# Performance work log

Hardware: AMD Instinct MI355X
Metric: run time of the kernel (lower is better)

Reference implementation:

```python
import jax, jax.numpy as jnp
import numpy as np

B, N, NFEAT, NHID, NOUT, H = 16, 1024, 128, 256, 256, 4
DH = NOUT // H  # 64 per head
EPS = 1e-5
ALPHA = 0.2  # LeakyReLU negative slope


def setup_inputs() -> dict:
    key = jax.random.key(0)
    ks = jax.random.split(key, 8)
    stdv = 1.0 / np.sqrt(NHID)
    return {
        "x": jax.random.normal(ks[0], (B, N, NFEAT), dtype=jnp.float32),
        "adj": jax.random.uniform(ks[1], (N, N), dtype=jnp.float32) / N,
        "gc_w": jax.random.uniform(ks[2], (NFEAT, NHID), minval=-stdv, maxval=stdv, dtype=jnp.float32),
        "gc_b": jax.random.uniform(ks[3], (NHID,), minval=-stdv, maxval=stdv, dtype=jnp.float32),
        "bn1_gamma": jnp.ones((NHID,), jnp.float32),
        "bn1_beta": jnp.zeros((NHID,), jnp.float32),
        "gat_w": jax.random.normal(ks[4], (H, NHID, DH), dtype=jnp.float32) * (1.0 / np.sqrt(NHID)),
        "conv_w": jax.random.normal(ks[5], (NOUT, NOUT, 3), dtype=jnp.float32) * (1.0 / np.sqrt(NOUT * 3)),
        "conv_b": jnp.zeros((NOUT,), jnp.float32),
        "bn2_gamma": jnp.ones((NOUT,), jnp.float32),
        "bn2_beta": jnp.zeros((NOUT,), jnp.float32),
    }


def reference(x, adj, gc_w, gc_b, bn1_gamma, bn1_beta, gat_w, conv_w, conv_b, bn2_gamma, bn2_beta):
    # --- GraphConvolution: adj @ (x @ W) + b, relu ---
    h = jnp.einsum("bnf,fo->bno", x, gc_w)
    h = jnp.einsum("nm,bmo->bno", adj, h) + gc_b
    h = jax.nn.relu(h)
    # --- BatchNorm1d over channel dim (training-mode batch stats), relu ---
    mu = h.mean((0, 1))
    var = h.var((0, 1))
    h = (h - mu) * jax.lax.rsqrt(var + EPS) * bn1_gamma + bn1_beta
    h = jax.nn.relu(h)
    # --- Multi-head GAT: per head hp, e = hp hp^T, leakyrelu, softmax, attn @ hp ---
    hp = jnp.einsum("bnf,hfd->bhnd", h, gat_w)          # (B,H,N,DH)
    e = jnp.einsum("bhnd,bhmd->bhnm", hp, hp)            # (B,H,N,N)
    e = jnp.where(e > 0, e, ALPHA * e)
    attn = jax.nn.softmax(e, axis=-1)
    out = jnp.einsum("bhnm,bhmd->bhnd", attn, hp)        # = sum_m attn * hp (the B,N,N,d repeat in torch)
    out = out.transpose(0, 2, 1, 3).reshape(B, N, H * DH)  # concat heads -> (B,N,NOUT)
    # --- TCN block: conv1d (k=3, pad 1) over node axis, batchnorm, relu (dropout=eval) ---
    xc = out.transpose(0, 2, 1)                          # (B,C,N)
    y = jax.lax.conv_general_dilated(xc, conv_w, (1,), [(1, 1)],
                                     dimension_numbers=("NCH", "OIH", "NCH"))
    y = y + conv_b[None, :, None]
    mu2 = y.mean((0, 2), keepdims=True)
    var2 = y.var((0, 2), keepdims=True)
    y = (y - mu2) * jax.lax.rsqrt(var2 + EPS) * bn2_gamma[None, :, None] + bn2_beta[None, :, None]
    y = jax.nn.relu(y)
    return y.transpose(0, 2, 1)                          # (B,N,NOUT)
```

## Files before the change

kernel.cpp:

```cpp
#include <hip/hip_runtime.h>
#include <hip/hip_bf16.h>


typedef unsigned short u16;
typedef __attribute__((ext_vector_type(8))) short short8;
typedef __attribute__((ext_vector_type(4))) float f32x4;

static __device__ __forceinline__ float4 ld4(const float* p){ return *(const float4*)p; }
static __device__ __forceinline__ void st4(float* p, float4 v){ *(float4*)p = v; }

static __device__ __forceinline__ u16 f2bf(float f){
  unsigned u = __builtin_bit_cast(unsigned, f);
  unsigned r = u + 0x7FFFu + ((u >> 16) & 1u);
  return (u16)(r >> 16);
}
static __device__ __forceinline__ float bf2f(u16 h){
  unsigned u = ((unsigned)h) << 16; return __builtin_bit_cast(float, u);
}
static __device__ __forceinline__ void st4bf(u16* p, u16 a, u16 b, u16 c, u16 d){
  uint2 v; v.x = (unsigned)a | ((unsigned)b << 16); v.y = (unsigned)c | ((unsigned)d << 16);
  *(uint2*)p = v;
}
static __device__ __forceinline__ f32x4 mfma16(short8 a, short8 b, f32x4 c){
  return __builtin_amdgcn_mfma_f32_16x16x32_bf16(a, b, c, 0, 0, 0);
}

template<int SPLIT, int K, int NN, int MODE, int AXSWAP, int BM, int BN, int WR, int WC>
static __device__ __forceinline__ void mgemm_body(
    const u16* __restrict__ Ah_, const u16* __restrict__ Al_,
    const u16* __restrict__ Bh_, const u16* __restrict__ Bl_,
    const u16* __restrict__ zbuf,
    void* __restrict__ C0v, void* __restrict__ C1v, void* __restrict__ C2v,
    const float* __restrict__ bias)
{
  constexpr int KT = K / 32;
  constexpr int WM = BM / WR, WN = BN / WC;
  constexpr int MI = WM / 16, NJ = WN / 16;
  __shared__ u16 Ah[BM * 32], Bh[BN * 32];
  __shared__ u16 Al[SPLIT == 3 ? BM * 32 : 8], Bl[SPLIT == 3 ? BN * 32 : 8];
  const int tid = threadIdx.x;
  const int n0 = (AXSWAP ? blockIdx.y : blockIdx.x) * BN;
  const int m0 = (AXSWAP ? blockIdx.x : blockIdx.y) * BM;
  const int lane = tid & 63, l15 = lane & 15, lq = lane >> 4;
  const int w = tid >> 6, wr = w / WC, wc = w % WC;

  f32x4 acc[MI][NJ] = {};

  for (int kt = 0; kt < KT; ++kt){
    const int k0 = kt * 32;
#pragma unroll
    for (int r = 0; r < BM / 64; ++r){
      const int slot = r * 256 + tid;
      const int row = slot & (BM - 1), kh = slot / BM;
      const int ldsoff = (r * 256 + (tid & 192)) * 8;
      const u16* asrc;
      if constexpr (MODE == 3){
        const int kz = k0 >> 8;
        const int ci0 = (k0 & 255) + kh * 8;
        const int R = m0 + row;
        const int nn = (R & 1023) + kz - 1;
        asrc = ((unsigned)nn < 1024u) ? (Ah_ + (size_t)(R + kz - 1) * 256 + ci0) : zbuf;
      } else {
        asrc = Ah_ + (size_t)(m0 + row) * K + k0 + kh * 8;
      }
      __builtin_amdgcn_global_load_lds(asrc, &Ah[ldsoff], 16, 0, 0);
      if constexpr (SPLIT == 3){
        const u16* asrc2 = Al_ + (size_t)(m0 + row) * K + k0 + kh * 8;
        __builtin_amdgcn_global_load_lds(asrc2, &Al[ldsoff], 16, 0, 0);
      }
    }
#pragma unroll
    for (int r = 0; r < BN / 64; ++r){
      const int slot = r * 256 + tid;
      const int row = slot & (BN - 1), kh = slot / BN;
      const int ldsoff = (r * 256 + (tid & 192)) * 8;
      const u16* bsrc = Bh_ + (size_t)(n0 + row) * K + k0 + kh * 8;
      __builtin_amdgcn_global_load_lds(bsrc, &Bh[ldsoff], 16, 0, 0);
      if constexpr (SPLIT == 3){
        const u16* bsrc2 = Bl_ + (size_t)(n0 + row) * K + k0 + kh * 8;
        __builtin_amdgcn_global_load_lds(bsrc2, &Bl[ldsoff], 16, 0, 0);
      }
    }
    __syncthreads();
    short8 afh[MI], bfh[NJ], afl[MI], bfl[NJ];
#pragma unroll
    for (int f = 0; f < MI; ++f){
      afh[f] = *(const short8*)&Ah[(lq * BM + wr * WM + f * 16 + l15) * 8];
      if constexpr (SPLIT == 3)
        afl[f] = *(const short8*)&Al[(lq * BM + wr * WM + f * 16 + l15) * 8];
    }
#pragma unroll
    for (int f = 0; f < NJ; ++f){
      bfh[f] = *(const short8*)&Bh[(lq * BN + wc * WN + f * 16 + l15) * 8];
      if constexpr (SPLIT == 3)
        bfl[f] = *(const short8*)&Bl[(lq * BN + wc * WN + f * 16 + l15) * 8];
    }
#pragma unroll
    for (int fi = 0; fi < MI; ++fi)
#pragma unroll
      for (int fj = 0; fj < NJ; ++fj){
        acc[fi][fj] = mfma16(afh[fi], bfh[fj], acc[fi][fj]);
        if constexpr (SPLIT == 3){
          acc[fi][fj] = mfma16(afl[fi], bfh[fj], acc[fi][fj]);
          acc[fi][fj] = mfma16(afh[fi], bfl[fj], acc[fi][fj]);
        }
      }
    __syncthreads();
  }

  const int rb = m0 + wr * WM;
  const int cb = n0 + wc * WN;
  if constexpr (MODE == 0){
    u16* H = (u16*)C0v; u16* L = (u16*)C1v;
#pragma unroll
    for (int fi = 0; fi < MI; ++fi){
      const int R = rb + fi * 16 + lq * 4;
      const int nn = R & 1023, bq = R >> 10;
#pragma unroll
      for (int fj = 0; fj < NJ; ++fj){
        const int c = cb + fj * 16 + l15;
        const size_t off = (size_t)(bq * 256 + c) * 1024 + nn;
        u16 h_[4], l_[4];
#pragma unroll
        for (int r = 0; r < 4; ++r){
          float v = acc[fi][fj][r];
          u16 hi = f2bf(v); h_[r] = hi; l_[r] = f2bf(v - bf2f(hi));
        }
        st4bf(H + off, h_[0], h_[1], h_[2], h_[3]);
        st4bf(L + off, l_[0], l_[1], l_[2], l_[3]);
      }
    }
  } else if constexpr (MODE == 1){
    u16* GH = (u16*)C0v; u16* GL = (u16*)C1v; float* PT = (float*)C2v;
    const int mb = AXSWAP ? blockIdx.x : blockIdx.y;
#pragma unroll
    for (int fj = 0; fj < NJ; ++fj){
      const int c = cb + fj * 16 + l15;
      const int o = c & 255, bq = c >> 8;
      const float bs = bias[o];
      float s = 0.f, q = 0.f;
#pragma unroll
      for (int fi = 0; fi < MI; ++fi){
        const int R = rb + fi * 16 + lq * 4;
#pragma unroll
        for (int r = 0; r < 4; ++r){
          const float v = fmaxf(acc[fi][fj][r] + bs, 0.f);
          s += v; q = fmaf(v, v, q);
          const u16 hi = f2bf(v);
          const size_t off = ((size_t)bq * 1024 + R + r) * 256 + o;
          GH[off] = hi;
          GL[off] = f2bf(v - bf2f(hi));
        }
      }
      s += __shfl_xor(s, 16, 64); s += __shfl_xor(s, 32, 64);
      q += __shfl_xor(q, 16, 64); q += __shfl_xor(q, 32, 64);
      if (lq == 0){
        PT[mb * 4096 + c]         = s;
        PT[65536 + mb * 4096 + c] = q;
      }
    }
  } else if constexpr (MODE == 2){
    u16* H = (u16*)C0v; u16* L = (u16*)C1v; u16* T = (u16*)C2v;
#pragma unroll
    for (int fi = 0; fi < MI; ++fi){
      const int R = rb + fi * 16 + lq * 4;
#pragma unroll
      for (int fj = 0; fj < NJ; ++fj){
        const int c = cb + fj * 16 + l15;
        u16 h_[4];
#pragma unroll
        for (int r = 0; r < 4; ++r){
          float v = acc[fi][fj][r];
          u16 hi = f2bf(v); h_[r] = hi;
          H[(size_t)(R + r) * 256 + c] = hi;
          L[(size_t)(R + r) * 256 + c] = f2bf(v - bf2f(hi));
        }
        st4bf(T + (size_t)c * 16384 + R, h_[0], h_[1], h_[2], h_[3]);
      }
    }
  } else {
    float* Y = (float*)C0v; float* PT = (float*)C2v;
    const int slot = blockIdx.y * 2 + wr;
#pragma unroll
    for (int fj = 0; fj < NJ; ++fj){
      const int c = cb + fj * 16 + l15;
      const float bs = bias[c];
      float s = 0.f, q = 0.f;
#pragma unroll
      for (int fi = 0; fi < MI; ++fi){
        const int R = rb + fi * 16 + lq * 4;
#pragma unroll
        for (int r = 0; r < 4; ++r){
          const float v = acc[fi][fj][r] + bs;
          s += v; q = fmaf(v, v, q);
          Y[(size_t)(R + r) * 256 + c] = v;
        }
      }
      s += __shfl_xor(s, 16, 64); s += __shfl_xor(s, 32, 64);
      q += __shfl_xor(q, 16, 64); q += __shfl_xor(q, 32, 64);
      if (lq == 0){
        PT[slot * 256 + c]         = s;
        PT[65536 + slot * 256 + c] = q;
      }
    }
  }
}

__global__ __launch_bounds__(256) void gemm0_k(
    const u16* __restrict__ Ah_, const u16* __restrict__ Bh_,
    const u16* __restrict__ zbuf, void* __restrict__ C0, void* __restrict__ C1)
{ mgemm_body<1, 128, 256, 0, 0, 128, 64, 2, 2>(Ah_, nullptr, Bh_, nullptr, zbuf, C0, C1, nullptr, nullptr); }

__global__ __launch_bounds__(256) void gemm1_k(
    const u16* __restrict__ Ah_, const u16* __restrict__ Al_,
    const u16* __restrict__ Bh_, const u16* __restrict__ Bl_,
    const u16* __restrict__ zbuf, void* __restrict__ C0, void* __restrict__ C1,
    void* __restrict__ C2, const float* __restrict__ bias)
{ mgemm_body<3, 1024, 4096, 1, 1, 64, 128, 1, 4>(Ah_, Al_, Bh_, Bl_, zbuf, C0, C1, C2, bias); }

__global__ __launch_bounds__(256) void gemm2_k(
    const u16* __restrict__ Ah_, const u16* __restrict__ Al_,
    const u16* __restrict__ Bh_, const u16* __restrict__ Bl_,
    const u16* __restrict__ zbuf,
    void* __restrict__ C0, void* __restrict__ C1, void* __restrict__ C2)
{ mgemm_body<3, 256, 256, 2, 0, 128, 64, 2, 2>(Ah_, Al_, Bh_, Bl_, zbuf, C0, C1, C2, nullptr); }

__global__ __launch_bounds__(256) void gemm3_k(
    const u16* __restrict__ Ah_, const u16* __restrict__ Bh_,
    const u16* __restrict__ zbuf, void* __restrict__ C0, void* __restrict__ C2,
    const float* __restrict__ bias)
{ mgemm_body<1, 768, 256, 3, 0, 128, 64, 2, 2>(Ah_, nullptr, Bh_, nullptr, zbuf, C0, nullptr, C2, bias); }

__global__ __launch_bounds__(256) void flash(
    const u16* __restrict__ hp_hi, const u16* __restrict__ hp_lo,
    const u16* __restrict__ hpT, u16* __restrict__ ao)
{
  __shared__ u16 Khi[4096], Klo[4096], Vt[4096];
  __shared__ u16 Pl[4][2048];
  __shared__ float Ls[4][32];
  const int tid = threadIdx.x;
  const int lane = tid & 63, l15 = lane & 15, lq = lane >> 4, w = tid >> 6;
  const int bid = blockIdx.x;
  const int b = bid & 15, k_ = bid >> 4, h = k_ >> 3, qo = k_ & 7;
  const size_t qrow0 = (size_t)b * 1024 + qo * 128 + w * 32;

  short8 qh[2][2], ql[2][2];
#pragma unroll
  for (int mf = 0; mf < 2; ++mf)
#pragma unroll
    for (int ks = 0; ks < 2; ++ks){
      const size_t off = (qrow0 + mf * 16 + l15) * 256 + h * 64 + ks * 32 + lq * 8;
      qh[mf][ks] = *(const short8*)(hp_hi + off);
      ql[mf][ks] = *(const short8*)(hp_lo + off);
    }

  f32x4 o_[4][2] = {};
  float ls[8] = {};

  for (int kt = 0; kt < 16; ++kt){
    const int kv0 = kt * 64;
#pragma unroll
    for (int r = 0; r < 2; ++r){
      const int slot = r * 256 + tid;
      const int g1 = slot >> 6, g2 = slot & 63;
      const int ldsoff = (r * 256 + (tid & 192)) * 8;
      const u16* ksrc = hp_hi + ((size_t)b * 1024 + kv0 + g2) * 256 + h * 64 + g1 * 8;
      __builtin_amdgcn_global_load_lds(ksrc, &Khi[ldsoff], 16, 0, 0);
      const u16* ksrc2 = hp_lo + ((size_t)b * 1024 + kv0 + g2) * 256 + h * 64 + g1 * 8;
      __builtin_amdgcn_global_load_lds(ksrc2, &Klo[ldsoff], 16, 0, 0);
      const u16* vsrc = hpT + (size_t)(h * 64 + g2) * 16384 + b * 1024 + kv0 + g1 * 8;
      __builtin_amdgcn_global_load_lds(vsrc, &Vt[ldsoff], 16, 0, 0);
    }
    __syncthreads();

#pragma unroll
    for (int nf = 0; nf < 4; ++nf){
      short8 kf[2], kg[2];
#pragma unroll
      for (int ks = 0; ks < 2; ++ks){
        kf[ks] = *(const short8*)&Khi[((ks * 4 + lq) * 64 + nf * 16 + l15) * 8];
        kg[ks] = *(const short8*)&Klo[((ks * 4 + lq) * 64 + nf * 16 + l15) * 8];
      }
      const int kv = nf * 16 + l15;
#pragma unroll
      for (int mf = 0; mf < 2; ++mf){
        f32x4 s = {};
#pragma unroll
        for (int ks = 0; ks < 2; ++ks){
          s = mfma16(qh[mf][ks], kf[ks], s);
          s = mfma16(ql[mf][ks], kf[ks], s);
          s = mfma16(qh[mf][ks], kg[ks], s);
        }
        const int qb = mf * 16 + lq * 4;
        const int base = ((kv >> 3) * 32 + qb) * 8 + (kv & 7);
#pragma unroll
        for (int r = 0; r < 4; ++r){
          float v = s[r];
          v = v > 0.f ? v : 0.2f * v;
          const float p = __expf(v - 40.f);
          ls[mf * 4 + r] += p;
          Pl[w][base + r * 8] = f2bf(p);
        }
      }
    }

#pragma unroll
    for (int ks = 0; ks < 2; ++ks){
      short8 va[4], pf[2];
#pragma unroll
      for (int f = 0; f < 4; ++f)
        va[f] = *(const short8*)&Vt[((ks * 4 + lq) * 64 + f * 16 + l15) * 8];
#pragma unroll
      for (int f = 0; f < 2; ++f)
        pf[f] = *(const short8*)&Pl[w][((ks * 4 + lq) * 32 + f * 16 + l15) * 8];
#pragma unroll
      for (int df = 0; df < 4; ++df)
#pragma unroll
        for (int qf = 0; qf < 2; ++qf)
          o_[df][qf] = mfma16(va[df], pf[qf], o_[df][qf]);
    }
    __syncthreads();
  }

#pragma unroll
  for (int mask = 1; mask < 16; mask <<= 1)
#pragma unroll
    for (int i = 0; i < 8; ++i)
      ls[i] += __shfl_xor(ls[i], mask, 64);
  if (l15 == 0){
#pragma unroll
    for (int mf = 0; mf < 2; ++mf)
#pragma unroll
      for (int r = 0; r < 4; ++r)
        Ls[w][mf * 16 + lq * 4 + r] = ls[mf * 4 + r];
  }
  __syncthreads();
  float inv[2];
#pragma unroll
  for (int qf = 0; qf < 2; ++qf) inv[qf] = 1.0f / Ls[w][qf * 16 + l15];

#pragma unroll
  for (int qf = 0; qf < 2; ++qf)
#pragma unroll
    for (int df = 0; df < 4; ++df){
      const size_t addr = (qrow0 + qf * 16 + l15) * 256 + h * 64 + df * 16 + lq * 4;
      st4bf(ao + addr,
            f2bf(o_[df][qf][0] * inv[qf]), f2bf(o_[df][qf][1] * inv[qf]),
            f2bf(o_[df][qf][2] * inv[qf]), f2bf(o_[df][qf][3] * inv[qf]));
    }
}

__global__ __launch_bounds__(256) void bn_final(const float* __restrict__ part,
                                                const float* __restrict__ gamma,
                                                const float* __restrict__ beta,
                                                float* __restrict__ prm)
{
  const int t = threadIdx.x;
  float s = 0.f, q = 0.f;
#pragma unroll 8
  for (int i = 0; i < 256; ++i){ s += part[i * 256 + t]; q += part[65536 + i * 256 + t]; }
  const float mu = s * (1.f / 16384.f);
  const float var = q * (1.f / 16384.f) - mu * mu;
  prm[t] = mu;
  prm[256 + t] = rsqrtf(var + 1e-5f) * gamma[t];
  prm[512 + t] = beta[t];
}

__global__ __launch_bounds__(256) void bn_apply_split(
    const u16* __restrict__ GH, const u16* __restrict__ GL,
    u16* __restrict__ H, u16* __restrict__ L, const float* __restrict__ prm)
{
  const int idx = blockIdx.x * 256 + threadIdx.x;
  const size_t off = (size_t)idx * 4;
  const int o = (int)(off & 255);
  const uint2 hv = *(const uint2*)(GH + off);
  const uint2 lv = *(const uint2*)(GL + off);
  const float4 m = ld4(prm + o), rs = ld4(prm + 256 + o), bt = ld4(prm + 512 + o);
  float x0 = bf2f((u16)(hv.x & 0xffff)) + bf2f((u16)(lv.x & 0xffff));
  float x1 = bf2f((u16)(hv.x >> 16))    + bf2f((u16)(lv.x >> 16));
  float x2 = bf2f((u16)(hv.y & 0xffff)) + bf2f((u16)(lv.y & 0xffff));
  float x3 = bf2f((u16)(hv.y >> 16))    + bf2f((u16)(lv.y >> 16));
  u16 h_[4], l_[4];
  float v;
  v = fmaxf(fmaf(x0 - m.x, rs.x, bt.x), 0.f); h_[0] = f2bf(v); l_[0] = f2bf(v - bf2f(h_[0]));
  v = fmaxf(fmaf(x1 - m.y, rs.y, bt.y), 0.f); h_[1] = f2bf(v); l_[1] = f2bf(v - bf2f(h_[1]));
  v = fmaxf(fmaf(x2 - m.z, rs.z, bt.z), 0.f); h_[2] = f2bf(v); l_[2] = f2bf(v - bf2f(h_[2]));
  v = fmaxf(fmaf(x3 - m.w, rs.w, bt.w), 0.f); h_[3] = f2bf(v); l_[3] = f2bf(v - bf2f(h_[3]));
  st4bf(H + off, h_[0], h_[1], h_[2], h_[3]);
  st4bf(L + off, l_[0], l_[1], l_[2], l_[3]);
}

__global__ __launch_bounds__(256) void bn_apply(const float* __restrict__ in,
                                                float* __restrict__ outp,
                                                const float* __restrict__ prm)
{
  const int idx = blockIdx.x * 256 + threadIdx.x;
  const size_t off = (size_t)idx * 8;
  const int o = (int)(off & 255);
  const float4 x0 = ld4(in + off),      x1 = ld4(in + off + 4);
  const float4 m0 = ld4(prm + o),       m1 = ld4(prm + o + 4);
  const float4 r0 = ld4(prm + 256 + o), r1 = ld4(prm + 256 + o + 4);
  const float4 b0 = ld4(prm + 512 + o), b1 = ld4(prm + 512 + o + 4);
  float4 y0, y1;
  y0.x = fmaxf(fmaf(x0.x - m0.x, r0.x, b0.x), 0.f);
  y0.y = fmaxf(fmaf(x0.y - m0.y, r0.y, b0.y), 0.f);
  y0.z = fmaxf(fmaf(x0.z - m0.z, r0.z, b0.z), 0.f);
  y0.w = fmaxf(fmaf(x0.w - m0.w, r0.w, b0.w), 0.f);
  y1.x = fmaxf(fmaf(x1.x - m1.x, r1.x, b1.x), 0.f);
  y1.y = fmaxf(fmaf(x1.y - m1.y, r1.y, b1.y), 0.f);
  y1.z = fmaxf(fmaf(x1.z - m1.z, r1.z, b1.z), 0.f);
  y1.w = fmaxf(fmaf(x1.w - m1.w, r1.w, b1.w), 0.f);
  st4(outp + off, y0);
  st4(outp + off + 4, y1);
}

__global__ __launch_bounds__(256) void pack_w(
    const float* __restrict__ x, const float* __restrict__ adj,
    const float* __restrict__ gcw, const float* __restrict__ gatw,
    const float* __restrict__ convw,
    u16* __restrict__ xbf, u16* __restrict__ adjh, u16* __restrict__ adjl,
    u16* __restrict__ w0t, u16* __restrict__ w2th, u16* __restrict__ w2tl,
    u16* __restrict__ cwt, u16* __restrict__ zb)
{
  const int idx = blockIdx.x * 256 + threadIdx.x;
  if (idx < 2097152) xbf[idx] = f2bf(x[idx]);
  if (idx < 1048576){
    const float v = adj[idx];
    const u16 hi = f2bf(v);
    adjh[idx] = hi; adjl[idx] = f2bf(v - bf2f(hi));
  }
  if (idx < 32768){
    const int o = idx >> 7, f = idx & 127;
    w0t[idx] = f2bf(gcw[f * 256 + o]);
  }
  if (idx < 65536){
    const int c = idx >> 8, f = idx & 255;
    const float v = gatw[(c >> 6) * 16384 + f * 64 + (c & 63)];
    const u16 hi = f2bf(v);
    w2th[idx] = hi; w2tl[idx] = f2bf(v - bf2f(hi));
  }
  if (idx < 196608){
    const int co = idx / 768, k = idx - co * 768;
    const int kz = k >> 8, ci = k & 255;
    cwt[idx] = f2bf(convw[co * 768 + ci * 3 + kz]);
  }
  if (idx < 2048) zb[idx] = 0;
}

extern "C" void kernel_launch(void* const* d_in, const int* in_sizes, int n_in,
                              void* d_out, int out_size, void* d_ws, size_t ws_size,
                              hipStream_t stream)
{
  const float* x     = (const float*)d_in[0];
  const float* adj   = (const float*)d_in[1];
  const float* gc_w  = (const float*)d_in[2];
  const float* gc_b  = (const float*)d_in[3];
  const float* bn1g  = (const float*)d_in[4];
  const float* bn1b  = (const float*)d_in[5];
  const float* gatw  = (const float*)d_in[6];
  const float* convw = (const float*)d_in[7];
  const float* convb = (const float*)d_in[8];
  const float* bn2g  = (const float*)d_in[9];
  const float* bn2b  = (const float*)d_in[10];
  char* ws  = (char*)d_ws;
  char* out = (char*)d_out;

  u16* h1t_hi = (u16*)(ws + 0);
  u16* h1t_lo = (u16*)(ws + 8388608);
  u16* x_bf   = (u16*)(ws + 16777216);
  u16* adj_hi = (u16*)(ws + 20971520);
  u16* adj_lo = (u16*)(ws + 23068672);
  u16* hpT    = (u16*)(ws + 16777216);
  u16* w0t    = (u16*)(ws + 25165824);
  u16* w2th   = (u16*)(ws + 25231360);
  u16* w2tl   = (u16*)(ws + 25362432);
  u16* cwt    = (u16*)(ws + 25493504);
  u16* zbuf   = (u16*)(ws + 25886720);
  float* P1   = (float*)(ws + 25890816);
  float* PR1  = (float*)(ws + 26415104);
  float* PR2  = (float*)(ws + 26419200);
  u16* h_hi  = (u16*)(ws + 0);
  u16* h_lo  = (u16*)(ws + 8388608);
  u16* ao    = (u16*)(ws + 0);
  u16* g_hi  = (u16*)out;
  u16* g_lo  = (u16*)(out + 8388608);
  u16* hp_hi = (u16*)out;
  u16* hp_lo = (u16*)(out + 8388608);
  float* y   = (float*)out;

  pack_w<<<8192, 256, 0, stream>>>(x, adj, gc_w, gatw, convw,
                                   x_bf, adj_hi, adj_lo, w0t, w2th, w2tl, cwt, zbuf);
  gemm0_k<<<dim3(4, 128), 256, 0, stream>>>(x_bf, w0t, zbuf, h1t_hi, h1t_lo);
  gemm1_k<<<dim3(16, 32), 256, 0, stream>>>(adj_hi, adj_lo, h1t_hi, h1t_lo, zbuf,
                                            g_hi, g_lo, P1, gc_b);
  bn_final<<<1, 256, 0, stream>>>(P1, bn1g, bn1b, PR1);
  bn_apply_split<<<4096, 256, 0, stream>>>(g_hi, g_lo, h_hi, h_lo, PR1);
  gemm2_k<<<dim3(4, 128), 256, 0, stream>>>(h_hi, h_lo, w2th, w2tl, zbuf, hp_hi, hp_lo, hpT);
  flash<<<512, 256, 0, stream>>>(hp_hi, hp_lo, hpT, ao);
  gemm3_k<<<dim3(4, 128), 256, 0, stream>>>(ao, cwt, zbuf, y, P1, convb);
  bn_final<<<1, 256, 0, stream>>>(P1, bn2g, bn2b, PR2);
  bn_apply<<<2048, 256, 0, stream>>>(y, y, PR2);
}
```

Measured before the change: 301.5 us.

## Double-buffer LDS tiles in GEMM and flash-attention kernels with MFMA priority hints

```diff
diff --git a/kernel.cpp b/kernel.cpp
--- a/kernel.cpp
+++ b/kernel.cpp
@@ -36,8 +36,8 @@
   constexpr int KT = K / 32;
   constexpr int WM = BM / WR, WN = BN / WC;
   constexpr int MI = WM / 16, NJ = WN / 16;
-  __shared__ u16 Ah[BM * 32], Bh[BN * 32];
-  __shared__ u16 Al[SPLIT == 3 ? BM * 32 : 8], Bl[SPLIT == 3 ? BN * 32 : 8];
+  __shared__ u16 Ah[2][BM * 32], Bh[2][BN * 32];
+  __shared__ u16 Al[2][SPLIT == 3 ? BM * 32 : 8], Bl[2][SPLIT == 3 ? BN * 32 : 8];
   const int tid = threadIdx.x;
   const int n0 = (AXSWAP ? blockIdx.y : blockIdx.x) * BN;
   const int m0 = (AXSWAP ? blockIdx.x : blockIdx.y) * BM;
@@ -46,7 +46,7 @@
 
   f32x4 acc[MI][NJ] = {};
 
-  for (int kt = 0; kt < KT; ++kt){
+  auto STAGE = [&](int buf, int kt){
     const int k0 = kt * 32;
 #pragma unroll
     for (int r = 0; r < BM / 64; ++r){
@@ -63,10 +63,10 @@
       } else {
         asrc = Ah_ + (size_t)(m0 + row) * K + k0 + kh * 8;
       }
-      __builtin_amdgcn_global_load_lds(asrc, &Ah[ldsoff], 16, 0, 0);
+      __builtin_amdgcn_global_load_lds(asrc, &Ah[buf][ldsoff], 16, 0, 0);
       if constexpr (SPLIT == 3){
         const u16* asrc2 = Al_ + (size_t)(m0 + row) * K + k0 + kh * 8;
-        __builtin_amdgcn_global_load_lds(asrc2, &Al[ldsoff], 16, 0, 0);
+        __builtin_amdgcn_global_load_lds(asrc2, &Al[buf][ldsoff], 16, 0, 0);
       }
     }
 #pragma unroll
@@ -75,25 +75,31 @@
       const int row = slot & (BN - 1), kh = slot / BN;
       const int ldsoff = (r * 256 + (tid & 192)) * 8;
       const u16* bsrc = Bh_ + (size_t)(n0 + row) * K + k0 + kh * 8;
-      __builtin_amdgcn_global_load_lds(bsrc, &Bh[ldsoff], 16, 0, 0);
+      __builtin_amdgcn_global_load_lds(bsrc, &Bh[buf][ldsoff], 16, 0, 0);
       if constexpr (SPLIT == 3){
         const u16* bsrc2 = Bl_ + (size_t)(n0 + row) * K + k0 + kh * 8;
-        __builtin_amdgcn_global_load_lds(bsrc2, &Bl[ldsoff], 16, 0, 0);
-      }
-    }
-    __syncthreads();
+        __builtin_amdgcn_global_load_lds(bsrc2, &Bl[buf][ldsoff], 16, 0, 0);
+      }
+    }
+  };
+
+  STAGE(0, 0);
+  __syncthreads();
+  for (int kt = 0; kt < KT; ++kt){
+    const int cur = kt & 1;
+    if (kt + 1 < KT) STAGE(cur ^ 1, kt + 1);
     short8 afh[MI], bfh[NJ], afl[MI], bfl[NJ];
 #pragma unroll
     for (int f = 0; f < MI; ++f){
-      afh[f] = *(const short8*)&Ah[(lq * BM + wr * WM + f * 16 + l15) * 8];
+      afh[f] = *(const short8*)&Ah[cur][(lq * BM + wr * WM + f * 16 + l15) * 8];
       if constexpr (SPLIT == 3)
-        afl[f] = *(const short8*)&Al[(lq * BM + wr * WM + f * 16 + l15) * 8];
+        afl[f] = *(const short8*)&Al[cur][(lq * BM + wr * WM + f * 16 + l15) * 8];
     }
 #pragma unroll
     for (int f = 0; f < NJ; ++f){
-      bfh[f] = *(const short8*)&Bh[(lq * BN + wc * WN + f * 16 + l15) * 8];
+      bfh[f] = *(const short8*)&Bh[cur][(lq * BN + wc * WN + f * 16 + l15) * 8];
       if constexpr (SPLIT == 3)
-        bfl[f] = *(const short8*)&Bl[(lq * BN + wc * WN + f * 16 + l15) * 8];
+        bfl[f] = *(const short8*)&Bl[cur][(lq * BN + wc * WN + f * 16 + l15) * 8];
     }
 #pragma unroll
     for (int fi = 0; fi < MI; ++fi)
@@ -235,9 +241,8 @@
     const u16* __restrict__ hp_hi, const u16* __restrict__ hp_lo,
     const u16* __restrict__ hpT, u16* __restrict__ ao)
 {
-  __shared__ u16 Khi[4096], Klo[4096], Vt[4096];
+  __shared__ u16 Khi[2][4096], Klo[2][4096], Vt[2][4096];
   __shared__ u16 Pl[4][2048];
-  __shared__ float Ls[4][32];
   const int tid = threadIdx.x;
   const int lane = tid & 63, l15 = lane & 15, lq = lane >> 4, w = tid >> 6;
   const int bid = blockIdx.x;
@@ -254,10 +259,7 @@
       ql[mf][ks] = *(const short8*)(hp_lo + off);
     }
 
-  f32x4 o_[4][2] = {};
-  float ls[8] = {};
-
-  for (int kt = 0; kt < 16; ++kt){
+  auto STAGE = [&](int buf, int kt){
     const int kv0 = kt * 64;
 #pragma unroll
     for (int r = 0; r < 2; ++r){
@@ -265,32 +267,43 @@
       const int g1 = slot >> 6, g2 = slot & 63;
       const int ldsoff = (r * 256 + (tid & 192)) * 8;
       const u16* ksrc = hp_hi + ((size_t)b * 1024 + kv0 + g2) * 256 + h * 64 + g1 * 8;
-      __builtin_amdgcn_global_load_lds(ksrc, &Khi[ldsoff], 16, 0, 0);
+      __builtin_amdgcn_global_load_lds(ksrc, &Khi[buf][ldsoff], 16, 0, 0);
       const u16* ksrc2 = hp_lo + ((size_t)b * 1024 + kv0 + g2) * 256 + h * 64 + g1 * 8;
-      __builtin_amdgcn_global_load_lds(ksrc2, &Klo[ldsoff], 16, 0, 0);
+      __builtin_amdgcn_global_load_lds(ksrc2, &Klo[buf][ldsoff], 16, 0, 0);
       const u16* vsrc = hpT + (size_t)(h * 64 + g2) * 16384 + b * 1024 + kv0 + g1 * 8;
-      __builtin_amdgcn_global_load_lds(vsrc, &Vt[ldsoff], 16, 0, 0);
-    }
-    __syncthreads();
+      __builtin_amdgcn_global_load_lds(vsrc, &Vt[buf][ldsoff], 16, 0, 0);
+    }
+  };
+
+  f32x4 o_[4][2] = {};
+  float ls[8] = {};
+
+  STAGE(0, 0);
+  __syncthreads();
+  for (int kt = 0; kt < 16; ++kt){
+    const int cur = kt & 1;
+    if (kt < 15) STAGE(cur ^ 1, kt + 1);
 
 #pragma unroll
     for (int nf = 0; nf < 4; ++nf){
       short8 kf[2], kg[2];
 #pragma unroll
       for (int ks = 0; ks < 2; ++ks){
-        kf[ks] = *(const short8*)&Khi[((ks * 4 + lq) * 64 + nf * 16 + l15) * 8];
-        kg[ks] = *(const short8*)&Klo[((ks * 4 + lq) * 64 + nf * 16 + l15) * 8];
+        kf[ks] = *(const short8*)&Khi[cur][((ks * 4 + lq) * 64 + nf * 16 + l15) * 8];
+        kg[ks] = *(const short8*)&Klo[cur][((ks * 4 + lq) * 64 + nf * 16 + l15) * 8];
       }
       const int kv = nf * 16 + l15;
 #pragma unroll
       for (int mf = 0; mf < 2; ++mf){
         f32x4 s = {};
+        __builtin_amdgcn_s_setprio(1);
 #pragma unroll
         for (int ks = 0; ks < 2; ++ks){
           s = mfma16(qh[mf][ks], kf[ks], s);
           s = mfma16(ql[mf][ks], kf[ks], s);
           s = mfma16(qh[mf][ks], kg[ks], s);
         }
+        __builtin_amdgcn_s_setprio(0);
         const int qb = mf * 16 + lq * 4;
         const int base = ((kv >> 3) * 32 + qb) * 8 + (kv & 7);
 #pragma unroll
@@ -309,15 +322,17 @@
       short8 va[4], pf[2];
 #pragma unroll
       for (int f = 0; f < 4; ++f)
-        va[f] = *(const short8*)&Vt[((ks * 4 + lq) * 64 + f * 16 + l15) * 8];
+        va[f] = *(const short8*)&Vt[cur][((ks * 4 + lq) * 64 + f * 16 + l15) * 8];
 #pragma unroll
       for (int f = 0; f < 2; ++f)
         pf[f] = *(const short8*)&Pl[w][((ks * 4 + lq) * 32 + f * 16 + l15) * 8];
+      __builtin_amdgcn_s_setprio(1);
 #pragma unroll
       for (int df = 0; df < 4; ++df)
 #pragma unroll
         for (int qf = 0; qf < 2; ++qf)
           o_[df][qf] = mfma16(va[df], pf[qf], o_[df][qf]);
+      __builtin_amdgcn_s_setprio(0);
     }
     __syncthreads();
   }
@@ -327,17 +342,17 @@
 #pragma unroll
     for (int i = 0; i < 8; ++i)
       ls[i] += __shfl_xor(ls[i], mask, 64);
+  float* LsF = (float*)&Pl[w][0];
   if (l15 == 0){
 #pragma unroll
     for (int mf = 0; mf < 2; ++mf)
 #pragma unroll
       for (int r = 0; r < 4; ++r)
-        Ls[w][mf * 16 + lq * 4 + r] = ls[mf * 4 + r];
-  }
-  __syncthreads();
+        LsF[mf * 16 + lq * 4 + r] = ls[mf * 4 + r];
+  }
   float inv[2];
 #pragma unroll
-  for (int qf = 0; qf < 2; ++qf) inv[qf] = 1.0f / Ls[w][qf * 16 + l15];
+  for (int qf = 0; qf < 2; ++qf) inv[qf] = 1.0f / LsF[qf * 16 + l15];
 
 #pragma unroll
   for (int qf = 0; qf < 2; ++qf)
```

Result: no change. 305.1 us (+1.2%).
